# Kernel optimization log

Measured on AMD Instinct MI355X. Metric: run time of the kernel, lower is better.

## Reference

```python
import jax, jax.numpy as jnp
import numpy as np
import math

LEVEL_DIMS = [256, 512, 1024, 2048]
B, P, K, D = 8192, 64, 8, 512
EPS = 1e-5  # torch LayerNorm default eps


def _layernorm(x, g, b):
    m = jnp.mean(x, axis=-1, keepdims=True)
    v = jnp.var(x, axis=-1, keepdims=True)
    return (x - m) / jnp.sqrt(v + EPS) * g + b


def _l2norm(x):
    # F.normalize(dim=-1): x / max(||x||_2, 1e-12)
    n = jnp.sqrt(jnp.sum(x * x, axis=-1, keepdims=True))
    return x / jnp.maximum(n, 1e-12)


def setup_inputs() -> dict:
    key = jax.random.key(0)
    ks = iter(jax.random.split(key, 32))
    inp = {}
    for i, dim in enumerate(LEVEL_DIMS):
        inp[f'pooled_{i}'] = jax.random.normal(next(ks), (B, dim), jnp.float32)
        inp[f'proto_{i}'] = jax.random.normal(next(ks), (P, dim), jnp.float32)
        inp[f'ln_g_{i}'] = jnp.ones((2 * dim,), jnp.float32)
        inp[f'ln_b_{i}'] = jnp.zeros((2 * dim,), jnp.float32)
        inp[f'W_{i}'] = jax.random.normal(next(ks), (2 * dim, D), jnp.float32) * (1.0 / math.sqrt(2 * dim))
        inp[f'b_{i}'] = jnp.zeros((D,), jnp.float32)
    inp['text_base'] = jax.random.normal(next(ks), (K, D), jnp.float32)
    inp['logit_scale'] = jnp.ones((1,), jnp.float32)
    return inp


def reference(pooled_0, pooled_1, pooled_2, pooled_3,
              proto_0, proto_1, proto_2, proto_3,
              ln_g_0, ln_g_1, ln_g_2, ln_g_3,
              ln_b_0, ln_b_1, ln_b_2, ln_b_3,
              W_0, W_1, W_2, W_3,
              b_0, b_1, b_2, b_3,
              text_base, logit_scale):
    pooled = [pooled_0, pooled_1, pooled_2, pooled_3]
    proto = [proto_0, proto_1, proto_2, proto_3]
    ln_g = [ln_g_0, ln_g_1, ln_g_2, ln_g_3]
    ln_b = [ln_b_0, ln_b_1, ln_b_2, ln_b_3]
    Ws = [W_0, W_1, W_2, W_3]
    bs = [b_0, b_1, b_2, b_3]

    # text encoder: CLIP embeddings normalized, text_proj=Identity, normalized again (idempotent)
    text_features = _l2norm(text_base)  # [K, D]

    ctxs = []
    for pl, pr, g, bb, W, b in zip(pooled, proto, ln_g, ln_b, Ws, bs):
        proto_ctx = jnp.broadcast_to(jnp.mean(pr, axis=0, keepdims=True), pl.shape)  # [B, C]
        fused = jnp.concatenate([pl, proto_ctx], axis=1)  # [B, 2C]
        h = jax.nn.relu(_layernorm(fused, g, bb) @ W + b)  # [B, D]
        ctxs.append(_l2norm(h))
    image_contexts = jnp.stack(ctxs, axis=1)  # [B, L, D]

    logits = jnp.einsum('kd,bld->bkl', text_features, image_contexts)
    logits = logits / math.sqrt(D)
    logits = logits * jnp.clip(logit_scale, 1e-4, None)
    return jax.nn.softmax(logits, axis=-1)  # [B, K, L]
```

## Files before the change

### kernel.cpp

```cpp
#include <hip/hip_runtime.h>
#include <stdint.h>

typedef __bf16 bf16x8 __attribute__((ext_vector_type(8)));
typedef float f32x4 __attribute__((ext_vector_type(4)));

#define OFF_GWT   62914560u
#define OFF_H     66846720u
#define OFF_U     100679680u
#define OFF_GG    100687872u
#define OFF_BB    100696064u
#define OFF_SCAL  100704256u
#define WS_TOTAL  100719872u

__host__ __device__ __forceinline__ size_t gwt_off(int l) {
  return (size_t)262144u * (size_t)((1u << l) - 1u);
}

__device__ __forceinline__ unsigned short f2bf(float x) {
  return (unsigned short)((__float_as_uint(x) + 0x8000u) >> 16);
}
__device__ __forceinline__ unsigned pack2(float a, float b) {
  return ((__float_as_uint(a) + 0x8000u) >> 16) |
         ((__float_as_uint(b) + 0x8000u) & 0xffff0000u);
}
__device__ __forceinline__ void async_load16(const void* g, void* l) {
  __builtin_amdgcn_global_load_lds((const __attribute__((address_space(1))) void*)g,
                                   (__attribute__((address_space(3))) void*)l,
                                   16, 0, 0);
}

struct PrepArgs {
  const float* pooled[4];
  const float* proto[4];
  const float* W[4];
  const float* g[4];
  const float* beta[4];
  const float* bias[4];
  const float* text;
  const float* lsc;
  char* ws;
};

__global__ __launch_bounds__(256) void wtrans(PrepArgs A) {
  __shared__ unsigned short tile[128][66];
  __shared__ float redG[4][128], redB[4][128], redU[4][128];
  __shared__ float gsh[64], bsh[64], psh[64];
  __shared__ float redP[4][64];
  int t = threadIdx.x, bid = blockIdx.x;
  int l, idl;
  if (bid < 256)      { l = 3; idl = bid; }
  else if (bid < 384) { l = 2; idl = bid - 256; }
  else if (bid < 448) { l = 1; idl = bid - 384; }
  else                { l = 0; idl = bid - 448; }
  int C = 256 << l;
  int sid = idl >> 2, dchunk = idl & 3;
  int j0 = sid * 64, d0 = dchunk * 128;
  bool top = (j0 < C);
  int w = t >> 6, L = t & 63;
  float* scal = (float*)(A.ws + OFF_SCAL);

  if (t < 64) {
    gsh[t] = A.g[l][j0 + t];
    bsh[t] = A.beta[l][j0 + t];
  }
  if (!top) {
    const float* pr = A.proto[l];
    int cb0 = j0 - C;
    float s = 0.f;
#pragma unroll
    for (int r = 0; r < 16; ++r) s += pr[(size_t)(w * 16 + r) * C + cb0 + L];
    redP[w][L] = s;
  }
  __syncthreads();
  if (!top) {
    if (t < 64) {
      float pmv = (redP[0][t] + redP[1][t] + redP[2][t] + redP[3][t]) * (1.0f / 64.0f);
      psh[t] = pmv * gsh[t];
      if (dchunk == 0) {
        float s1 = pmv, s2 = pmv * pmv;
#pragma unroll
        for (int off = 1; off < 64; off <<= 1) {
          s1 += __shfl_xor(s1, off);
          s2 += __shfl_xor(s2, off);
        }
        if (t == 0) {
          atomicAdd(&scal[l], s1);
          atomicAdd(&scal[4 + l], s2);
        }
      }
    }
    __syncthreads();
  }

  const float* W = A.W[l];
  float2 v[16];
#pragma unroll
  for (int r = 0; r < 16; ++r) {
    int j = j0 + w * 16 + r;
    v[r] = *(const float2*)(W + (size_t)j * 512 + d0 + 2 * L);
  }
  float gp0 = 0.f, gp1 = 0.f, bp0 = 0.f, bp1 = 0.f, up0 = 0.f, up1 = 0.f;
#pragma unroll
  for (int r = 0; r < 16; ++r) {
    int jl = w * 16 + r;
    float g = gsh[jl], b = bsh[jl];
    gp0 = fmaf(g, v[r].x, gp0); gp1 = fmaf(g, v[r].y, gp1);
    bp0 = fmaf(b, v[r].x, bp0); bp1 = fmaf(b, v[r].y, bp1);
    if (top) {
      tile[2 * L][jl] = f2bf(g * v[r].x);
      tile[2 * L + 1][jl] = f2bf(g * v[r].y);
    } else {
      float p = psh[jl];
      up0 = fmaf(p, v[r].x, up0); up1 = fmaf(p, v[r].y, up1);
    }
  }
  redG[w][2 * L] = gp0; redG[w][2 * L + 1] = gp1;
  redB[w][2 * L] = bp0; redB[w][2 * L + 1] = bp1;
  if (!top) { redU[w][2 * L] = up0; redU[w][2 * L + 1] = up1; }
  __syncthreads();

  if (t < 128) {
    int d = l * 512 + d0 + t;
    float G = redG[0][t] + redG[1][t] + redG[2][t] + redG[3][t];
    float B = redB[0][t] + redB[1][t] + redB[2][t] + redB[3][t];
    atomicAdd(&((float*)(A.ws + OFF_GG))[d], G);
    atomicAdd(&((float*)(A.ws + OFF_BB))[d], B);
    if (!top) {
      float U = redU[0][t] + redU[1][t] + redU[2][t] + redU[3][t];
      atomicAdd(&((float*)(A.ws + OFF_U))[d], U);
    }
  }
  if (top) {
    unsigned short* gwT = (unsigned short*)(A.ws + OFF_GWT + gwt_off(l));
    int d = t >> 1, jh = (t & 1) * 32;
    const unsigned* trow = (const unsigned*)&tile[d][jh];
    uint4 q0 = make_uint4(trow[0], trow[1], trow[2], trow[3]);
    uint4 q1 = make_uint4(trow[4], trow[5], trow[6], trow[7]);
    uint4 q2 = make_uint4(trow[8], trow[9], trow[10], trow[11]);
    uint4 q3 = make_uint4(trow[12], trow[13], trow[14], trow[15]);
    uint4* dst = (uint4*)(gwT + (size_t)(d0 + d) * C + j0 + jh);
    dst[0] = q0; dst[1] = q1; dst[2] = q2; dst[3] = q3;
  }
}

struct G2Args {
  char* ws;
  const float* pooled[4];
  const float* bias[4];
};

__global__ __launch_bounds__(256, 3) void gemm2(G2Args A) {
  __shared__ __align__(16) char lds[18944];
  char* ws = A.ws;
  int t = threadIdx.x, bid = blockIdx.x;
  int l = 3 - (bid >> 8);
  int rb = (bid >> 2) & 63, cb = bid & 3;
  int C = 256 << l;
  int m0 = rb * 128, n0 = cb * 128;

  float* uArr  = (float*)(lds + 16384);
  float* gArr  = (float*)(lds + 16896);
  float* bArr  = (float*)(lds + 17408);
  float* rowM  = (float*)(lds + 17920);
  float* rowIS = (float*)(lds + 18432);
  const float* scal = (const float*)(ws + OFF_SCAL);

  if (t < 128) {
    int idx = l * 512 + n0 + t;
    uArr[t] = ((const float*)(ws + OFF_U))[idx];
    gArr[t] = ((const float*)(ws + OFF_GG))[idx];
    bArr[t] = ((const float*)(ws + OFF_BB))[idx] + A.bias[l][n0 + t];
  }

  int w = t >> 6, lane = t & 63, quad = lane >> 4, lc = lane & 15;
  const char* Bw = ws + OFF_GWT + gwt_off(l);
  const char* bP[2]; char* bD[2];
#pragma unroll
  for (int i = 0; i < 2; ++i) {
    int li = i * 256 + t;
    int rr = li >> 2, kq = li & 3;
    bP[i] = Bw + ((size_t)(n0 + rr) * C + kq * 8) * 2;
    bD[i] = lds + 8192 + i * 4096 + w * 1024;
  }
  int rA = t >> 2, kq = t & 3;
  const float* aG0 = A.pooled[l] + (size_t)(m0 + rA) * C + kq * 8;
  const float* aG1 = aG0 + (size_t)64 * C;
  int gsw = kq ^ ((rA >> 1) & 3);
  char* aW0 = lds + rA * 64 + gsw * 16;
  char* aW1 = aW0 + 64 * 64;
  int wr = (w >> 1) * 64, wc = (w & 1) * 64;
  int ag = quad ^ (((wr + lc) >> 1) & 3);
  const char* aF = lds + (wr + lc) * 64 + ag * 16;
  const char* bF = lds + 8192 + (wc + lc) * 64 + quad * 16;

  f32x4 acc[4][4] = {};
  float s1a = 0.f, s2a = 0.f, s1b = 0.f, s2b = 0.f;
  f32x4 a0 = *(const f32x4*)aG0, a1 = *(const f32x4*)(aG0 + 4);
  f32x4 a2 = *(const f32x4*)aG1, a3 = *(const f32x4*)(aG1 + 4);
  for (int k0 = 0; k0 < C; k0 += 32) {
    if (k0) __syncthreads();
    async_load16(bP[0], bD[0]); async_load16(bP[1], bD[1]);
    bP[0] += 64; bP[1] += 64;
    *(uint4*)aW0 = make_uint4(pack2(a0[0], a0[1]), pack2(a0[2], a0[3]),
                              pack2(a1[0], a1[1]), pack2(a1[2], a1[3]));
    *(uint4*)aW1 = make_uint4(pack2(a2[0], a2[1]), pack2(a2[2], a2[3]),
                              pack2(a3[0], a3[1]), pack2(a3[2], a3[3]));
    s1a += ((a0[0] + a0[1]) + (a0[2] + a0[3])) + ((a1[0] + a1[1]) + (a1[2] + a1[3]));
    s2a = fmaf(a0[0], a0[0], s2a); s2a = fmaf(a0[1], a0[1], s2a);
    s2a = fmaf(a0[2], a0[2], s2a); s2a = fmaf(a0[3], a0[3], s2a);
    s2a = fmaf(a1[0], a1[0], s2a); s2a = fmaf(a1[1], a1[1], s2a);
    s2a = fmaf(a1[2], a1[2], s2a); s2a = fmaf(a1[3], a1[3], s2a);
    s1b += ((a2[0] + a2[1]) + (a2[2] + a2[3])) + ((a3[0] + a3[1]) + (a3[2] + a3[3]));
    s2b = fmaf(a2[0], a2[0], s2b); s2b = fmaf(a2[1], a2[1], s2b);
    s2b = fmaf(a2[2], a2[2], s2b); s2b = fmaf(a2[3], a2[3], s2b);
    s2b = fmaf(a3[0], a3[0], s2b); s2b = fmaf(a3[1], a3[1], s2b);
    s2b = fmaf(a3[2], a3[2], s2b); s2b = fmaf(a3[3], a3[3], s2b);
    __syncthreads();
    if (k0 + 32 < C) {
      aG0 += 32; aG1 += 32;
      a0 = *(const f32x4*)aG0; a1 = *(const f32x4*)(aG0 + 4);
      a2 = *(const f32x4*)aG1; a3 = *(const f32x4*)(aG1 + 4);
    }
    __builtin_amdgcn_sched_barrier(0);
    bf16x8 av[4];
#pragma unroll
    for (int rt = 0; rt < 4; ++rt) av[rt] = *(const bf16x8*)(aF + rt * 1024);
#pragma unroll
    for (int ct = 0; ct < 4; ++ct) {
      bf16x8 bv = *(const bf16x8*)(bF + ct * 1024);
#pragma unroll
      for (int rt = 0; rt < 4; ++rt)
        acc[rt][ct] = __builtin_amdgcn_mfma_f32_16x16x32_bf16(av[rt], bv, acc[rt][ct], 0, 0, 0);
    }
  }

#pragma unroll
  for (int off = 1; off < 4; off <<= 1) {
    s1a += __shfl_xor(s1a, off); s2a += __shfl_xor(s2a, off);
    s1b += __shfl_xor(s1b, off); s2b += __shfl_xor(s2b, off);
  }
  if ((t & 3) == 0) {
    float inv2C = 1.0f / (float)(2 * C);
    float spro = scal[l], sqpro = scal[4 + l];
    float mra = (s1a + spro) * inv2C;
    rowM[rA] = mra;
    rowIS[rA] = rsqrtf((s2a + sqpro) * inv2C - mra * mra + 1e-5f);
    float mrb = (s1b + spro) * inv2C;
    rowM[64 + rA] = mrb;
    rowIS[64 + rA] = rsqrtf((s2b + sqpro) * inv2C - mrb * mrb + 1e-5f);
  }
  __syncthreads();

  char* Hl = ws + OFF_H + (size_t)l * 8388608;
#pragma unroll
  for (int rt = 0; rt < 4; ++rt) {
#pragma unroll
    for (int ct = 0; ct < 4; ++ct) {
      int nl = wc + ct * 16 + lc;
      float uu = uArr[nl], gg = gArr[nl], bb = bArr[nl];
      f32x4 a = acc[rt][ct];
#pragma unroll
      for (int reg = 0; reg < 4; ++reg) {
        int ml = wr + rt * 16 + quad * 4 + reg;
        float h = fmaf(a[reg] + uu - rowM[ml] * gg, rowIS[ml], bb);
        h = fmaxf(h, 0.f);
        float hp = __shfl_xor(h, 1);
        if (!(lc & 1)) {
          unsigned pkv = pack2(h, hp);
          *(unsigned*)(Hl + ((size_t)(m0 + ml) * 512 + n0 + nl) * 2) = pkv;
        }
      }
    }
  }
}

__global__ __launch_bounds__(256) void postK(const char* ws, const float* text,
                                             const float* lsc, float* out) {
  __shared__ float textL[4096];
  int t = threadIdx.x, b = blockIdx.x;
  {
    int gq = t >> 5, lq = t & 31;
    float v[16];
    float pa = 0.f;
#pragma unroll
    for (int i = 0; i < 16; ++i) {
      v[i] = text[gq * 512 + lq + 32 * i];
      pa = fmaf(v[i], v[i], pa);
    }
#pragma unroll
    for (int off = 1; off < 32; off <<= 1) pa += __shfl_xor(pa, off);
    float inv = 1.0f / fmaxf(sqrtf(pa), 1e-12f);
#pragma unroll
    for (int i = 0; i < 16; ++i) textL[gq * 512 + lq + 32 * i] = v[i] * inv;
  }
  __syncthreads();
  float scale = fmaxf(lsc[0], 1e-4f) * 0.04419417382415922f;
  int row = b * 16 + (t >> 4), q = t & 15;
  float lg[4][8];
#pragma unroll
  for (int l = 0; l < 4; ++l) {
    const uint4* hp = (const uint4*)(ws + OFF_H + (size_t)l * 8388608 +
                                     ((size_t)row * 512 + q * 32) * 2);
    float np = 0.f;
    float dp[8] = {};
#pragma unroll
    for (int ch = 0; ch < 4; ++ch) {
      uint4 u = hp[ch];
      int d0 = q * 32 + ch * 8;
      unsigned uw[4] = {u.x, u.y, u.z, u.w};
#pragma unroll
      for (int p = 0; p < 4; ++p) {
        float v0 = __uint_as_float(uw[p] << 16);
        float v1 = __uint_as_float(uw[p] & 0xffff0000u);
        int dd = d0 + p * 2;
        np = fmaf(v0, v0, np);
        np = fmaf(v1, v1, np);
#pragma unroll
        for (int k = 0; k < 8; ++k) {
          dp[k] = fmaf(v0, textL[k * 512 + dd], dp[k]);
          dp[k] = fmaf(v1, textL[k * 512 + dd + 1], dp[k]);
        }
      }
    }
#pragma unroll
    for (int off = 1; off < 16; off <<= 1) {
      np += __shfl_xor(np, off);
#pragma unroll
      for (int k = 0; k < 8; ++k) dp[k] += __shfl_xor(dp[k], off);
    }
    float innorm = scale / fmaxf(sqrtf(np), 1e-12f);
#pragma unroll
    for (int k = 0; k < 8; ++k) lg[l][k] = dp[k] * innorm;
  }
  if (q == 0) {
    float4* op = (float4*)out + (size_t)row * 8;
#pragma unroll
    for (int k = 0; k < 8; ++k) {
      float a = lg[0][k], b2 = lg[1][k], c = lg[2][k], d = lg[3][k];
      float mx = fmaxf(fmaxf(a, b2), fmaxf(c, d));
      float e0 = __expf(a - mx), e1 = __expf(b2 - mx);
      float e2 = __expf(c - mx), e3 = __expf(d - mx);
      float inv = 1.0f / (e0 + e1 + e2 + e3);
      op[k] = make_float4(e0 * inv, e1 * inv, e2 * inv, e3 * inv);
    }
  }
}

extern "C" void kernel_launch(void* const* d_in, const int* in_sizes, int n_in,
                              void* d_out, int out_size, void* d_ws, size_t ws_size,
                              hipStream_t stream) {
  (void)n_in; (void)out_size;
  if (ws_size < (size_t)WS_TOTAL) return;
  char* ws = (char*)d_ws;
  bool dict = (in_sizes[1] == 64 * 256);
  PrepArgs pa;
  for (int l = 0; l < 4; ++l) {
    if (dict) {
      pa.pooled[l] = (const float*)d_in[6 * l + 0];
      pa.proto[l]  = (const float*)d_in[6 * l + 1];
      pa.g[l]      = (const float*)d_in[6 * l + 2];
      pa.beta[l]   = (const float*)d_in[6 * l + 3];
      pa.W[l]      = (const float*)d_in[6 * l + 4];
      pa.bias[l]   = (const float*)d_in[6 * l + 5];
    } else {
      pa.pooled[l] = (const float*)d_in[l];
      pa.proto[l]  = (const float*)d_in[4 + l];
      pa.g[l]      = (const float*)d_in[8 + l];
      pa.beta[l]   = (const float*)d_in[12 + l];
      pa.W[l]      = (const float*)d_in[16 + l];
      pa.bias[l]   = (const float*)d_in[20 + l];
    }
  }
  pa.text = (const float*)d_in[24];
  pa.lsc = (const float*)d_in[25];
  pa.ws = ws;

  hipMemsetAsync(ws + OFF_U, 0, 3 * 8192 + 256, stream);
  wtrans<<<480, 256, 0, stream>>>(pa);

  G2Args g2;
  g2.ws = ws;
  for (int l = 0; l < 4; ++l) {
    g2.pooled[l] = pa.pooled[l];
    g2.bias[l] = pa.bias[l];
  }
  gemm2<<<1024, 256, 0, stream>>>(g2);
  postK<<<512, 256, 0, stream>>>(ws, pa.text, pa.lsc, (float*)d_out);
}
```

Before: 303.6 us.

## Double-buffer GEMM LDS tiles, remap block order, and restructure postK per-wave rows

The gemm2 main loop now keeps two LDS buffers for the A and B tiles, so the next k-slice is loaded and packed while MFMAs run on the current one. This leaves one barrier per iteration instead of two. The B tile also gets an XOR swizzle to avoid LDS bank conflicts, and block IDs are remapped so consecutive blocks interleave across levels for load balance. postK is rewritten to give one wave per row, with the normalized text held in registers instead of LDS and four times as many blocks. In exchange, gemm2 uses more LDS per block, which may lower occupancy, and postK adds longer shuffle reductions.

Result: slower. 407.4 us (+34.2%).

```diff
diff --git a/kernel.cpp b/kernel.cpp
--- a/kernel.cpp
+++ b/kernel.cpp
@@ -150,19 +150,21 @@
 };
 
 __global__ __launch_bounds__(256, 3) void gemm2(G2Args A) {
-  __shared__ __align__(16) char lds[18944];
+  __shared__ __align__(16) char lds[35328];
   char* ws = A.ws;
-  int t = threadIdx.x, bid = blockIdx.x;
+  int t = threadIdx.x;
+  int bid = ((blockIdx.x & 7) << 7) + (blockIdx.x >> 3);
   int l = 3 - (bid >> 8);
   int rb = (bid >> 2) & 63, cb = bid & 3;
   int C = 256 << l;
+  int nst = C >> 5;
   int m0 = rb * 128, n0 = cb * 128;
 
-  float* uArr  = (float*)(lds + 16384);
-  float* gArr  = (float*)(lds + 16896);
-  float* bArr  = (float*)(lds + 17408);
-  float* rowM  = (float*)(lds + 17920);
-  float* rowIS = (float*)(lds + 18432);
+  float* uArr  = (float*)(lds + 32768);
+  float* gArr  = (float*)(lds + 33280);
+  float* bArr  = (float*)(lds + 33792);
+  float* rowM  = (float*)(lds + 34304);
+  float* rowIS = (float*)(lds + 34816);
   const float* scal = (const float*)(ws + OFF_SCAL);
 
   if (t < 128) {
@@ -173,38 +175,38 @@
   }
 
   int w = t >> 6, lane = t & 63, quad = lane >> 4, lc = lane & 15;
+
   const char* Bw = ws + OFF_GWT + gwt_off(l);
-  const char* bP[2]; char* bD[2];
+  const char* bP[2];
 #pragma unroll
   for (int i = 0; i < 2; ++i) {
     int li = i * 256 + t;
-    int rr = li >> 2, kq = li & 3;
+    int rr = li >> 2, s = li & 3;
+    int kq = s ^ ((rr >> 1) & 3);
     bP[i] = Bw + ((size_t)(n0 + rr) * C + kq * 8) * 2;
-    bD[i] = lds + 8192 + i * 4096 + w * 1024;
-  }
-  int rA = t >> 2, kq = t & 3;
-  const float* aG0 = A.pooled[l] + (size_t)(m0 + rA) * C + kq * 8;
+  }
+  char* BD = lds + 16384 + w * 1024;
+
+  int rA = t >> 2, sA = t & 3;
+  int kqA = sA ^ ((rA >> 1) & 3);
+  const float* aG0 = A.pooled[l] + (size_t)(m0 + rA) * C + kqA * 8;
   const float* aG1 = aG0 + (size_t)64 * C;
-  int gsw = kq ^ ((rA >> 1) & 3);
-  char* aW0 = lds + rA * 64 + gsw * 16;
-  char* aW1 = aW0 + 64 * 64;
+  int aOff0 = rA * 64 + sA * 16;
+  int aOff1 = aOff0 + 4096;
+
   int wr = (w >> 1) * 64, wc = (w & 1) * 64;
-  int ag = quad ^ (((wr + lc) >> 1) & 3);
-  const char* aF = lds + (wr + lc) * 64 + ag * 16;
-  const char* bF = lds + 8192 + (wc + lc) * 64 + quad * 16;
-
-  f32x4 acc[4][4] = {};
+  int aFoff = (wr + lc) * 64 + (quad ^ (((wr + lc) >> 1) & 3)) * 16;
+  int bFoff = (wc + lc) * 64 + (quad ^ (((wc + lc) >> 1) & 3)) * 16;
+
+  f32x4 a0, a1, a2, a3;
   float s1a = 0.f, s2a = 0.f, s1b = 0.f, s2b = 0.f;
-  f32x4 a0 = *(const f32x4*)aG0, a1 = *(const f32x4*)(aG0 + 4);
-  f32x4 a2 = *(const f32x4*)aG1, a3 = *(const f32x4*)(aG1 + 4);
-  for (int k0 = 0; k0 < C; k0 += 32) {
-    if (k0) __syncthreads();
-    async_load16(bP[0], bD[0]); async_load16(bP[1], bD[1]);
-    bP[0] += 64; bP[1] += 64;
-    *(uint4*)aW0 = make_uint4(pack2(a0[0], a0[1]), pack2(a0[2], a0[3]),
-                              pack2(a1[0], a1[1]), pack2(a1[2], a1[3]));
-    *(uint4*)aW1 = make_uint4(pack2(a2[0], a2[1]), pack2(a2[2], a2[3]),
-                              pack2(a3[0], a3[1]), pack2(a3[2], a3[3]));
+  auto packA = [&](int buf) {
+    *(uint4*)(lds + buf * 8192 + aOff0) =
+        make_uint4(pack2(a0[0], a0[1]), pack2(a0[2], a0[3]),
+                   pack2(a1[0], a1[1]), pack2(a1[2], a1[3]));
+    *(uint4*)(lds + buf * 8192 + aOff1) =
+        make_uint4(pack2(a2[0], a2[1]), pack2(a2[2], a2[3]),
+                   pack2(a3[0], a3[1]), pack2(a3[2], a3[3]));
     s1a += ((a0[0] + a0[1]) + (a0[2] + a0[3])) + ((a1[0] + a1[1]) + (a1[2] + a1[3]));
     s2a = fmaf(a0[0], a0[0], s2a); s2a = fmaf(a0[1], a0[1], s2a);
     s2a = fmaf(a0[2], a0[2], s2a); s2a = fmaf(a0[3], a0[3], s2a);
@@ -215,13 +217,37 @@
     s2b = fmaf(a2[2], a2[2], s2b); s2b = fmaf(a2[3], a2[3], s2b);
     s2b = fmaf(a3[0], a3[0], s2b); s2b = fmaf(a3[1], a3[1], s2b);
     s2b = fmaf(a3[2], a3[2], s2b); s2b = fmaf(a3[3], a3[3], s2b);
-    __syncthreads();
-    if (k0 + 32 < C) {
-      aG0 += 32; aG1 += 32;
-      a0 = *(const f32x4*)aG0; a1 = *(const f32x4*)(aG0 + 4);
-      a2 = *(const f32x4*)aG1; a3 = *(const f32x4*)(aG1 + 4);
-    }
-    __builtin_amdgcn_sched_barrier(0);
+  };
+
+  async_load16(bP[0], BD);
+  async_load16(bP[1], BD + 4096);
+  bP[0] += 64; bP[1] += 64;
+  a0 = *(const f32x4*)aG0; a1 = *(const f32x4*)(aG0 + 4);
+  a2 = *(const f32x4*)aG1; a3 = *(const f32x4*)(aG1 + 4);
+  packA(0);
+  if (nst > 1) {
+    aG0 += 32; aG1 += 32;
+    a0 = *(const f32x4*)aG0; a1 = *(const f32x4*)(aG0 + 4);
+    a2 = *(const f32x4*)aG1; a3 = *(const f32x4*)(aG1 + 4);
+  }
+  __syncthreads();
+
+  f32x4 acc[4][4] = {};
+  for (int k = 0; k < nst; ++k) {
+    int cur = k & 1, nxt = cur ^ 1;
+    if (k + 1 < nst) {
+      async_load16(bP[0], BD + nxt * 8192);
+      async_load16(bP[1], BD + nxt * 8192 + 4096);
+      bP[0] += 64; bP[1] += 64;
+      packA(nxt);
+      if (k + 2 < nst) {
+        aG0 += 32; aG1 += 32;
+        a0 = *(const f32x4*)aG0; a1 = *(const f32x4*)(aG0 + 4);
+        a2 = *(const f32x4*)aG1; a3 = *(const f32x4*)(aG1 + 4);
+      }
+    }
+    const char* aF = lds + cur * 8192 + aFoff;
+    const char* bF = lds + 16384 + cur * 8192 + bFoff;
     bf16x8 av[4];
 #pragma unroll
     for (int rt = 0; rt < 4; ++rt) av[rt] = *(const bf16x8*)(aF + rt * 1024);
@@ -232,6 +258,7 @@
       for (int rt = 0; rt < 4; ++rt)
         acc[rt][ct] = __builtin_amdgcn_mfma_f32_16x16x32_bf16(av[rt], bv, acc[rt][ct], 0, 0, 0);
     }
+    __syncthreads();
   }
 
 #pragma unroll
@@ -276,54 +303,68 @@
 
 __global__ __launch_bounds__(256) void postK(const char* ws, const float* text,
                                              const float* lsc, float* out) {
-  __shared__ float textL[4096];
-  int t = threadIdx.x, b = blockIdx.x;
-  {
-    int gq = t >> 5, lq = t & 31;
-    float v[16];
-    float pa = 0.f;
-#pragma unroll
-    for (int i = 0; i < 16; ++i) {
-      v[i] = text[gq * 512 + lq + 32 * i];
-      pa = fmaf(v[i], v[i], pa);
-    }
-#pragma unroll
-    for (int off = 1; off < 32; off <<= 1) pa += __shfl_xor(pa, off);
-    float inv = 1.0f / fmaxf(sqrtf(pa), 1e-12f);
-#pragma unroll
-    for (int i = 0; i < 16; ++i) textL[gq * 512 + lq + 32 * i] = v[i] * inv;
-  }
-  __syncthreads();
+  int t = threadIdx.x, w = t >> 6, lane = t & 63;
+  int row = blockIdx.x * 4 + w;
+  int d0 = lane * 8;
+
+  f32x4 tr[16];
+#pragma unroll
+  for (int k = 0; k < 8; ++k) {
+    tr[2 * k]     = *(const f32x4*)(text + k * 512 + d0);
+    tr[2 * k + 1] = *(const f32x4*)(text + k * 512 + d0 + 4);
+  }
+  float nq[8];
+#pragma unroll
+  for (int k = 0; k < 8; ++k) {
+    f32x4 a = tr[2 * k], b = tr[2 * k + 1];
+    float s = 0.f;
+    s = fmaf(a[0], a[0], s); s = fmaf(a[1], a[1], s);
+    s = fmaf(a[2], a[2], s); s = fmaf(a[3], a[3], s);
+    s = fmaf(b[0], b[0], s); s = fmaf(b[1], b[1], s);
+    s = fmaf(b[2], b[2], s); s = fmaf(b[3], b[3], s);
+    nq[k] = s;
+  }
+#pragma unroll
+  for (int off = 1; off < 64; off <<= 1) {
+#pragma unroll
+    for (int k = 0; k < 8; ++k) nq[k] += __shfl_xor(nq[k], off);
+  }
+#pragma unroll
+  for (int k = 0; k < 8; ++k) {
+    float inv = 1.0f / fmaxf(sqrtf(nq[k]), 1e-12f);
+    tr[2 * k] *= inv;
+    tr[2 * k + 1] *= inv;
+  }
+
   float scale = fmaxf(lsc[0], 1e-4f) * 0.04419417382415922f;
-  int row = b * 16 + (t >> 4), q = t & 15;
   float lg[4][8];
 #pragma unroll
   for (int l = 0; l < 4; ++l) {
-    const uint4* hp = (const uint4*)(ws + OFF_H + (size_t)l * 8388608 +
-                                     ((size_t)row * 512 + q * 32) * 2);
+    uint4 u = *(const uint4*)(ws + OFF_H + (size_t)l * 8388608 +
+                              ((size_t)row * 512 + d0) * 2);
+    unsigned uw[4] = {u.x, u.y, u.z, u.w};
+    float v[8];
+#pragma unroll
+    for (int p = 0; p < 4; ++p) {
+      v[2 * p]     = __uint_as_float(uw[p] << 16);
+      v[2 * p + 1] = __uint_as_float(uw[p] & 0xffff0000u);
+    }
     float np = 0.f;
-    float dp[8] = {};
-#pragma unroll
-    for (int ch = 0; ch < 4; ++ch) {
-      uint4 u = hp[ch];
-      int d0 = q * 32 + ch * 8;
-      unsigned uw[4] = {u.x, u.y, u.z, u.w};
-#pragma unroll
-      for (int p = 0; p < 4; ++p) {
-        float v0 = __uint_as_float(uw[p] << 16);
-        float v1 = __uint_as_float(uw[p] & 0xffff0000u);
-        int dd = d0 + p * 2;
-        np = fmaf(v0, v0, np);
-        np = fmaf(v1, v1, np);
-#pragma unroll
-        for (int k = 0; k < 8; ++k) {
-          dp[k] = fmaf(v0, textL[k * 512 + dd], dp[k]);
-          dp[k] = fmaf(v1, textL[k * 512 + dd + 1], dp[k]);
-        }
-      }
-    }
-#pragma unroll
-    for (int off = 1; off < 16; off <<= 1) {
+#pragma unroll
+    for (int j = 0; j < 8; ++j) np = fmaf(v[j], v[j], np);
+    float dp[8];
+#pragma unroll
+    for (int k = 0; k < 8; ++k) {
+      f32x4 ta = tr[2 * k], tb = tr[2 * k + 1];
+      float d = 0.f;
+      d = fmaf(v[0], ta[0], d); d = fmaf(v[1], ta[1], d);
+      d = fmaf(v[2], ta[2], d); d = fmaf(v[3], ta[3], d);
+      d = fmaf(v[4], tb[0], d); d = fmaf(v[5], tb[1], d);
+      d = fmaf(v[6], tb[2], d); d = fmaf(v[7], tb[3], d);
+      dp[k] = d;
+    }
+#pragma unroll
+    for (int off = 1; off < 64; off <<= 1) {
       np += __shfl_xor(np, off);
 #pragma unroll
       for (int k = 0; k < 8; ++k) dp[k] += __shfl_xor(dp[k], off);
@@ -332,17 +373,14 @@
 #pragma unroll
     for (int k = 0; k < 8; ++k) lg[l][k] = dp[k] * innorm;
   }
-  if (q == 0) {
-    float4* op = (float4*)out + (size_t)row * 8;
-#pragma unroll
-    for (int k = 0; k < 8; ++k) {
-      float a = lg[0][k], b2 = lg[1][k], c = lg[2][k], d = lg[3][k];
-      float mx = fmaxf(fmaxf(a, b2), fmaxf(c, d));
-      float e0 = __expf(a - mx), e1 = __expf(b2 - mx);
-      float e2 = __expf(c - mx), e3 = __expf(d - mx);
-      float inv = 1.0f / (e0 + e1 + e2 + e3);
-      op[k] = make_float4(e0 * inv, e1 * inv, e2 * inv, e3 * inv);
-    }
+
+  if (lane < 8) {
+    float a = lg[0][lane], b2 = lg[1][lane], c = lg[2][lane], d = lg[3][lane];
+    float mx = fmaxf(fmaxf(a, b2), fmaxf(c, d));
+    float e0 = __expf(a - mx), e1 = __expf(b2 - mx);
+    float e2 = __expf(c - mx), e3 = __expf(d - mx);
+    float inv = 1.0f / (e0 + e1 + e2 + e3);
+    ((float4*)out)[(size_t)row * 8 + lane] = make_float4(e0 * inv, e1 * inv, e2 * inv, e3 * inv);
   }
 }
 
@@ -385,5 +423,5 @@
     g2.bias[l] = pa.bias[l];
   }
   gemm2<<<1024, 256, 0, stream>>>(g2);
-  postK<<<512, 256, 0, stream>>>(ws, pa.text, pa.lsc, (float*)d_out);
-}
+  postK<<<2048, 256, 0, stream>>>(ws, pa.text, pa.lsc, (float*)d_out);
+}
```
